# Optimization experiments

Hardware: AMD Instinct MI355X
Metric: run time of the kernel (lower is better)

Reference implementation:

```python
import jax, jax.numpy as jnp
import numpy as np

B, S, DIM, H, HD, K, DEPTH = 2, 2048, 512, 8, 64, 64, 8
SCALE = 1.0 / np.sqrt(HD)


def _cantor_coords(seq_len: int, depth: int) -> np.ndarray:
    # Vectorized port of CantorAttention._cantor_coordinate over all positions.
    x = np.arange(seq_len, dtype=np.float64) / max(1, seq_len - 1)
    x = np.clip(x, 1e-06, 1.0 - 1e-06)
    val = np.zeros(seq_len, dtype=np.float64)
    factor = 0.5
    for _ in range(depth):
        x *= 3.0
        digit = np.floor(x)
        x -= digit
        val += (digit == 2.0) * factor
        factor *= 0.5
    return val.astype(np.float32)


def _build_routes(seq_len: int, k: int, depth: int) -> np.ndarray:
    # k nearest neighbors in Cantor space (smallest |c_i - c_j|), per position.
    c = _cantor_coords(seq_len, depth)
    dist = np.abs(c[:, None] - c[None, :])  # (S, S) built once on host
    routes = np.argsort(dist, axis=1, kind='stable')[:, :k]  # ascending distance
    return routes.astype(np.int32)


def setup_inputs() -> dict:
    key = jax.random.key(0)
    k1, k2, k3 = jax.random.split(key, 3)
    x = jax.random.normal(k1, (B, S, DIM), dtype=jnp.float32)
    Wqkv = jax.random.normal(k2, (DIM, 3 * DIM), dtype=jnp.float32) * (1.0 / np.sqrt(DIM))
    bqkv = jnp.zeros((3 * DIM,), dtype=jnp.float32)
    Wout = jax.random.normal(k3, (DIM, DIM), dtype=jnp.float32) * (1.0 / np.sqrt(DIM))
    bout = jnp.zeros((DIM,), dtype=jnp.float32)
    routes = jnp.asarray(_build_routes(S, K, DEPTH))  # (S, K) int32
    return {"x": x, "Wqkv": Wqkv, "bqkv": bqkv, "Wout": Wout, "bout": bout, "routes": routes}


def reference(x, Wqkv, bqkv, Wout, bout, routes):
    b, s, _ = x.shape
    qkv = x @ Wqkv + bqkv  # (B, S, 3*DIM)
    qkv = qkv.reshape(b, s, 3, H, HD)
    q = jnp.transpose(qkv[:, :, 0], (0, 2, 1, 3))  # (B, H, S, HD)
    k = jnp.transpose(qkv[:, :, 1], (0, 2, 1, 3))
    v = jnp.transpose(qkv[:, :, 2], (0, 2, 1, 3))
    # Gather K/V along sequence dim by Cantor routes -> (B, H, S, K, HD)
    k_g = k[:, :, routes, :]
    v_g = v[:, :, routes, :]
    scores = jnp.einsum('bhsd,bhskd->bhsk', q, k_g) * SCALE
    w = jax.nn.softmax(scores, axis=-1)  # dropout disabled (eval)
    out = jnp.einsum('bhsk,bhskd->bhsd', w, v_g)  # (B, H, S, HD)
    out = jnp.transpose(out, (0, 2, 1, 3)).reshape(b, s, DIM)
    return out @ Wout + bout
```

## Files before the change

kernel.cpp:

```cpp
#include <hip/hip_runtime.h>
#include <math.h>

#define B_    2
#define S_    2048
#define DIM_  512
#define H_    8
#define HD_   64
#define K_    64
#define M_    (B_ * S_)
#define NQKV_ (3 * DIM_)

typedef __attribute__((ext_vector_type(8))) _Float16       half8;
typedef __attribute__((ext_vector_type(2))) _Float16       half2v;
typedef __attribute__((ext_vector_type(8))) unsigned short ushort8v;
typedef __attribute__((ext_vector_type(4))) float          float4v;

__device__ __forceinline__ unsigned short f2h(float f) {
    _Float16 h = (_Float16)f;
    unsigned short u; __builtin_memcpy(&u, &h, 2); return u;
}
__device__ __forceinline__ float h2f(unsigned short u) {
    _Float16 h; __builtin_memcpy(&h, &u, 2); return (float)h;
}

template<int CTRL>
__device__ __forceinline__ float dpp_addf(float x) {
    int y = __builtin_amdgcn_update_dpp(0, __builtin_bit_cast(int, x),
                                        CTRL, 0xF, 0xF, true);
    return x + __builtin_bit_cast(float, y);
}
template<int CTRL>
__device__ __forceinline__ float dpp_maxf(float x) {
    int y = __builtin_amdgcn_update_dpp(0, __builtin_bit_cast(int, x),
                                        CTRL, 0xF, 0xF, true);
    return fmaxf(x, __builtin_bit_cast(float, y));
}

__device__ __forceinline__ void load_lds16(const unsigned short* g, unsigned short* l) {
    __builtin_amdgcn_global_load_lds(
        (const __attribute__((address_space(1))) void*)g,
        (__attribute__((address_space(3))) void*)l, 16, 0, 0);
}

__global__ __launch_bounds__(256) void prep_all(
    const float* __restrict__ X, unsigned short* __restrict__ Xh,
    const float* __restrict__ Wq, unsigned short* __restrict__ Wqh,
    const float* __restrict__ Wo, unsigned short* __restrict__ Woh,
    const int* __restrict__ routes, int* __restrict__ members,
    int4* __restrict__ recs, int* __restrict__ nchp)
{
    __shared__ int smem[2048 * 3 + 256];
    const int bid = blockIdx.x, t = threadIdx.x;

    if (bid < 1024) {
        size_t i = ((size_t)bid * 256 + t) * 8;
        float4 a = *(const float4*)&X[i];
        float4 b = *(const float4*)&X[i + 4];
        float f[8] = {a.x, a.y, a.z, a.w, b.x, b.y, b.z, b.w};
        ushort8v h;
        #pragma unroll
        for (int j = 0; j < 8; ++j) h[j] = f2h(f[j]);
        *(ushort8v*)&Xh[i] = h;
        return;
    }

    if (bid == 2048) {
        int* cnt  = smem;
        int* base = smem + 2048;
        int* cur  = smem + 4096;
        int* ps   = smem + 6144;
        for (int i = t; i < 2048; i += 256) cnt[i] = 0;
        __syncthreads();
        int lead[8];
        #pragma unroll
        for (int i = 0; i < 8; ++i) {
            lead[i] = routes[(size_t)(i * 256 + t) * K_];
            atomicAdd(&cnt[lead[i]], 1);
        }
        __syncthreads();
        int loc[8], sum = 0;
        #pragma unroll
        for (int i = 0; i < 8; ++i) { loc[i] = sum; sum += cnt[t * 8 + i]; }
        ps[t] = sum;
        __syncthreads();
        for (int off = 1; off < 256; off <<= 1) {
            int v = ps[t];
            if (t >= off) v += ps[t - off];
            __syncthreads(); ps[t] = v; __syncthreads();
        }
        const int excl = ps[t] - sum;
        #pragma unroll
        for (int i = 0; i < 8; ++i) { base[t * 8 + i] = excl + loc[i]; cur[t * 8 + i] = 0; }
        __syncthreads();
        #pragma unroll
        for (int i = 0; i < 8; ++i) {
            int s = i * 256 + t;
            members[base[lead[i]] + atomicAdd(&cur[lead[i]], 1)] = s;
        }
        int cloc[8], csum = 0;
        #pragma unroll
        for (int i = 0; i < 8; ++i) { cloc[i] = csum; csum += (cnt[t * 8 + i] + 7) >> 3; }
        __syncthreads();
        ps[t] = csum;
        __syncthreads();
        for (int off = 1; off < 256; off <<= 1) {
            int v = ps[t];
            if (t >= off) v += ps[t - off];
            __syncthreads(); ps[t] = v; __syncthreads();
        }
        const int cexcl = ps[t] - csum;
        #pragma unroll
        for (int i = 0; i < 8; ++i) {
            const int c = t * 8 + i, n = cnt[c];
            int w0 = cexcl + cloc[i];
            for (int k = 0; k * 8 < n; ++k) {
                int rem = n - k * 8;
                recs[w0 + k] = make_int4(c, base[c] + k * 8, rem < 8 ? rem : 8, 0);
            }
        }
        if (t == 255) nchp[0] = ps[255];
        return;
    }

    float (*tile)[33] = (float (*)[33])smem;
    const float* W;
    unsigned short* Whi;
    int N, k0, n0;
    if (bid < 1792) {
        int idx = bid - 1024;
        W = Wq; Whi = Wqh; N = NQKV_;
        n0 = (idx % 48) * 32; k0 = (idx / 48) * 32;
    } else {
        int idx = bid - 1792;
        W = Wo; Whi = Woh; N = DIM_;
        n0 = (idx % 16) * 32; k0 = (idx / 16) * 32;
    }
    const int c = t & 31, r8 = t >> 5;
    #pragma unroll
    for (int i = 0; i < 4; ++i) {
        int r = r8 + i * 8;
        tile[r][c] = W[(size_t)(k0 + r) * N + n0 + c];
    }
    __syncthreads();
    #pragma unroll
    for (int i = 0; i < 4; ++i) {
        int r = r8 + i * 8;
        Whi[(size_t)(n0 + r) * 512 + k0 + c] = f2h(tile[c][r]);
    }
}

template<int BM, int BN, int WM, int WN, int TERMS>
__global__ __launch_bounds__(256) void gemm_mfma(
    const unsigned short* __restrict__ Ahi, const unsigned short* __restrict__ Alo,
    const unsigned short* __restrict__ Wh,
    const float* __restrict__ bias, float* __restrict__ C,
    unsigned short* __restrict__ Qho, unsigned short* __restrict__ Kho,
    unsigned short* __restrict__ Vho,
    int N, int Kd, int mode)
{
    constexpr int TM = WM / 16, TN = WN / 16;
    constexpr int WAVES_N = BN / WN;
    __shared__ unsigned short Ah[2][BM][32];
    __shared__ unsigned short Al[TERMS == 2 ? 2 : 1][TERMS == 2 ? BM : 1][32];
    __shared__ unsigned short Bh[2][BN][32];

    const int t = threadIdx.x, lane = t & 63, wave = t >> 6;
    const int wm = (wave / WAVES_N) * WM, wn = (wave % WAVES_N) * WN;
    const int m0 = blockIdx.y * BM, n0 = blockIdx.x * BN;
    const int l15 = lane & 15, l4 = lane >> 4;

    const int srow = lane >> 2;
    const int scol = (lane & 3) * 8;

    float4v acc[TM][TN];
    #pragma unroll
    for (int i = 0; i < TM; ++i)
        #pragma unroll
        for (int j = 0; j < TN; ++j)
            #pragma unroll
            for (int r = 0; r < 4; ++r) acc[i][j][r] = 0.f;

    const int NK = Kd / 32;

    #pragma unroll
    for (int c = wave; c < BM / 16; c += 4) {
        size_t g = (size_t)(m0 + c * 16 + srow) * Kd + scol;
        load_lds16(&Ahi[g], &Ah[0][c * 16][0]);
        if constexpr (TERMS == 2) load_lds16(&Alo[g], &Al[0][c * 16][0]);
    }
    #pragma unroll
    for (int c = wave; c < BN / 16; c += 4) {
        size_t g = (size_t)(n0 + c * 16 + srow) * Kd + scol;
        load_lds16(&Wh[g], &Bh[0][c * 16][0]);
    }
    __syncthreads();

    for (int ks = 0; ks < NK; ++ks) {
        const int cur = ks & 1, nxt = cur ^ 1;

        if (ks + 1 < NK) {
            const int k1 = (ks + 1) * 32;
            #pragma unroll
            for (int c = wave; c < BM / 16; c += 4) {
                size_t g = (size_t)(m0 + c * 16 + srow) * Kd + k1 + scol;
                load_lds16(&Ahi[g], &Ah[nxt][c * 16][0]);
                if constexpr (TERMS == 2) load_lds16(&Alo[g], &Al[nxt][c * 16][0]);
            }
            #pragma unroll
            for (int c = wave; c < BN / 16; c += 4) {
                size_t g = (size_t)(n0 + c * 16 + srow) * Kd + k1 + scol;
                load_lds16(&Wh[g], &Bh[nxt][c * 16][0]);
            }
        }

        half8 fa_h[TM], fa_l[TM], fb[TN];
        #pragma unroll
        for (int im = 0; im < TM; ++im) {
            fa_h[im] = *(const half8*)&Ah[cur][wm + im * 16 + l15][l4 * 8];
            if constexpr (TERMS == 2)
                fa_l[im] = *(const half8*)&Al[cur][wm + im * 16 + l15][l4 * 8];
        }
        #pragma unroll
        for (int in = 0; in < TN; ++in)
            fb[in] = *(const half8*)&Bh[cur][wn + in * 16 + l15][l4 * 8];
        #pragma unroll
        for (int im = 0; im < TM; ++im)
            #pragma unroll
            for (int in = 0; in < TN; ++in) {
                acc[im][in] = __builtin_amdgcn_mfma_f32_16x16x32_f16(fa_h[im], fb[in], acc[im][in], 0, 0, 0);
                if constexpr (TERMS == 2)
                    acc[im][in] = __builtin_amdgcn_mfma_f32_16x16x32_f16(fa_l[im], fb[in], acc[im][in], 0, 0, 0);
            }

        __syncthreads();
    }

    if (mode == 0) {
        #pragma unroll
        for (int in = 0; in < TN; ++in) {
            int n = n0 + wn + in * 16 + l15;
            float bv = bias[n];
            #pragma unroll
            for (int im = 0; im < TM; ++im) {
                int mb = m0 + wm + im * 16 + l4 * 4;
                #pragma unroll
                for (int r = 0; r < 4; ++r)
                    C[(size_t)(mb + r) * N + n] = acc[im][in][r] + bv;
            }
        }
    } else {
        #pragma unroll
        for (int in = 0; in < TN; ++in) {
            int n = n0 + wn + in * 16 + l15;
            int which = n >> 9, h = (n >> 6) & 7, d = n & 63;
            unsigned short* dst = (which == 0) ? Qho : (which == 1 ? Kho : Vho);
            float bv = bias[n];
            #pragma unroll
            for (int im = 0; im < TM; ++im) {
                int mb = m0 + wm + im * 16 + l4 * 4;
                #pragma unroll
                for (int r = 0; r < 4; ++r) {
                    int m = mb + r, b = m >> 11, s = m & 2047;
                    dst[(((size_t)b * H_ + h) * S_ + s) * HD_ + d] =
                        f2h(acc[im][in][r] + bv);
                }
            }
        }
    }
}

__global__ __launch_bounds__(256, 3) void attn_kernel(
    const unsigned short* __restrict__ Qh, const unsigned short* __restrict__ Kh,
    const unsigned short* __restrict__ Vh, const int* __restrict__ routes,
    const int* __restrict__ members, const int4* __restrict__ recs,
    const int* __restrict__ nchp,
    unsigned short* __restrict__ Oh)
{
    const int wv = threadIdx.x >> 6, lane = threadIdx.x & 63;
    const int p = lane & 7, jl = lane >> 3;

    const int unit = blockIdx.x * 4 + wv;
    const int bh = unit & 15, cidx = unit >> 4;
    const int b = bh >> 3, h = bh & 7;

    const unsigned short* qbase = Qh + (size_t)bh * S_ * HD_;
    const unsigned short* kbase = Kh + (size_t)bh * S_ * HD_;
    const unsigned short* vbase = Vh + (size_t)bh * S_ * HD_;
    const int nch = nchp[0];

    for (int chunk = cidx; chunk < nch; chunk += 512) {
        const int4 rec = recs[chunk];
        const int leader = rec.x, mstart = rec.y, mcnt = rec.z;

        const int rl = routes[(size_t)leader * K_ + lane];

        int mrow[8];
        #pragma unroll
        for (int r = 0; r < 8; ++r)
            mrow[r] = members[mstart + (r < mcnt ? r : 0)];

        ushort8v kreg[8];
        #pragma unroll
        for (int pass = 0; pass < 8; ++pass) {
            int rk = __shfl(rl, pass * 8 + jl);
            kreg[pass] = *(const ushort8v*)&kbase[(size_t)rk * HD_ + p * 8];
        }
        #pragma unroll
        for (int i = 0; i < 8; ++i) asm volatile("" : "+v"(kreg[i]));

        ushort8v vreg[8];
        #pragma unroll
        for (int i = 0; i < 8; ++i) {
            int rv = __shfl(rl, i * 8 + p);
            vreg[i] = *(const ushort8v*)&vbase[(size_t)rv * HD_ + jl * 8];
        }
        #pragma unroll
        for (int i = 0; i < 8; ++i) asm volatile("" : "+v"(vreg[i]));

        half2v q[8][4];
        #pragma unroll
        for (int r = 0; r < 8; ++r) {
            ushort8v qv = *(const ushort8v*)&qbase[(size_t)mrow[r] * HD_ + p * 8];
            __builtin_memcpy(&q[r][0], &qv, 16);
        }

        float sc[8] = {0.f,0.f,0.f,0.f,0.f,0.f,0.f,0.f};
        #pragma unroll
        for (int pass = 0; pass < 8; ++pass) {
            half2v kp[4];
            __builtin_memcpy(kp, &kreg[pass], 16);
            #pragma unroll
            for (int r = 0; r < 8; ++r) {
                float pa = 0.f;
                #pragma unroll
                for (int i = 0; i < 4; ++i)
                    pa = __builtin_amdgcn_fdot2(q[r][i], kp[i], pa, false);
                pa = dpp_addf<0xB1>(pa);
                pa = dpp_addf<0x4E>(pa);
                pa = dpp_addf<0x141>(pa);
                sc[r] = (pass == p) ? pa : sc[r];
            }
        }

        float w[8];
        #pragma unroll
        for (int r = 0; r < 8; ++r) {
            float s = sc[r] * 0.125f;
            float m = s;
            m = dpp_maxf<0xB1>(m);  m = dpp_maxf<0x4E>(m);
            m = dpp_maxf<0x141>(m); m = dpp_maxf<0x140>(m);
            m = fmaxf(m, __shfl_xor(m, 16));
            m = fmaxf(m, __shfl_xor(m, 32));
            float e = __expf(s - m);
            float su = e;
            su = dpp_addf<0xB1>(su);  su = dpp_addf<0x4E>(su);
            su = dpp_addf<0x141>(su); su = dpp_addf<0x140>(su);
            su += __shfl_xor(su, 16);
            su += __shfl_xor(su, 32);
            w[r] = e / su;
        }

        float vf[8][8];
        #pragma unroll
        for (int i = 0; i < 8; ++i)
            #pragma unroll
            for (int j = 0; j < 8; ++j) vf[i][j] = h2f(vreg[i][j]);

        #pragma unroll
        for (int r = 0; r < 8; ++r) {
            float ac[8] = {0.f,0.f,0.f,0.f,0.f,0.f,0.f,0.f};
            #pragma unroll
            for (int i = 0; i < 8; ++i) {
                float wj = __shfl(w[r], p * 8 + i);
                #pragma unroll
                for (int j = 0; j < 8; ++j) ac[j] += wj * vf[i][j];
            }
            #pragma unroll
            for (int j = 0; j < 8; ++j) {
                ac[j] = dpp_addf<0xB1>(ac[j]);
                ac[j] = dpp_addf<0x4E>(ac[j]);
                ac[j] = dpp_addf<0x141>(ac[j]);
            }
            if (p == 0 && r < mcnt) {
                ushort8v ho;
                #pragma unroll
                for (int j = 0; j < 8; ++j) ho[j] = f2h(ac[j]);
                *(ushort8v*)&Oh[((size_t)b * S_ + mrow[r]) * DIM_ + h * HD_ + jl * 8] = ho;
            }
        }
    }
}

extern "C" void kernel_launch(void* const* d_in, const int* in_sizes, int n_in,
                              void* d_out, int out_size, void* d_ws, size_t ws_size,
                              hipStream_t stream)
{
    const float* x      = (const float*)d_in[0];
    const float* Wqkv   = (const float*)d_in[1];
    const float* bqkv   = (const float*)d_in[2];
    const float* Wout   = (const float*)d_in[3];
    const float* bout   = (const float*)d_in[4];
    const int*   routes = (const int*)d_in[5];
    float* out = (float*)d_out;

    char* w = (char*)d_ws;
    unsigned short* Qh = (unsigned short*)(w);
    unsigned short* Kh = (unsigned short*)(w + (8u << 20));
    unsigned short* Vh = (unsigned short*)(w + (16u << 20));
    unsigned short* xh = (unsigned short*)(w + (24u << 20));
    unsigned short* ah = xh;
    unsigned short* wqh = (unsigned short*)(w + (32u << 20));
    unsigned short* woh = (unsigned short*)(w + (32u << 20) + 1572864u);
    int*  members = (int*)(w + (34u << 20));
    int4* recs    = (int4*)(w + (34u << 20) + 8192u);
    int*  nchp    = (int*)(w + (34u << 20) + 8192u + 32768u);

    dim3 blk(256);

    prep_all<<<dim3(2049), blk, 0, stream>>>(x, xh, Wqkv, wqh, Wout, woh,
                                             routes, members, recs, nchp);

    gemm_mfma<128, 96, 64, 48, 1><<<dim3(NQKV_ / 96, M_ / 128), blk, 0, stream>>>(
        xh, nullptr, wqh, bqkv, nullptr, Qh, Kh, Vh, NQKV_, DIM_, 1);

    attn_kernel<<<dim3(2048), blk, 0, stream>>>(Qh, Kh, Vh, routes,
                                                members, recs, nchp, ah);

    gemm_mfma<64, 64, 32, 32, 1><<<dim3(DIM_ / 64, M_ / 64), blk, 0, stream>>>(
        ah, nullptr, woh, bout, out, nullptr, nullptr, nullptr, DIM_, DIM_, 0);
}
```

Measured before the change: 132.7 us.

## Move gathered attention onto MFMA with 16-member chunks and LDS-staged V

The attention kernel now groups up to 16 queries that share a route leader into each chunk, instead of 8. QK^T and PV are computed with 16x16x32 f16 MFMA instructions in place of fdot2 with DPP reductions. The gathered V rows are staged into swizzled LDS through global_load_lds, the probabilities are redistributed with ds_bpermute, and the softmax scale is folded into Q in the QKV GEMM epilogue. The aim is to cut scalar ALU and cross-lane shuffle cost and halve the number of K/V gathers per query. In exchange it adds LDS use, raises the occupancy hint to 4, and writes the output as scattered 2-byte stores.

```diff
diff --git a/kernel.cpp b/kernel.cpp
--- a/kernel.cpp
+++ b/kernel.cpp
@@ -11,29 +11,18 @@
 #define NQKV_ (3 * DIM_)
 
 typedef __attribute__((ext_vector_type(8))) _Float16       half8;
-typedef __attribute__((ext_vector_type(2))) _Float16       half2v;
 typedef __attribute__((ext_vector_type(8))) unsigned short ushort8v;
 typedef __attribute__((ext_vector_type(4))) float          float4v;
+
+union H8 { half8 h; ushort8v u; unsigned int w[4]; };
 
 __device__ __forceinline__ unsigned short f2h(float f) {
     _Float16 h = (_Float16)f;
     unsigned short u; __builtin_memcpy(&u, &h, 2); return u;
 }
-__device__ __forceinline__ float h2f(unsigned short u) {
-    _Float16 h; __builtin_memcpy(&h, &u, 2); return (float)h;
-}
-
-template<int CTRL>
-__device__ __forceinline__ float dpp_addf(float x) {
-    int y = __builtin_amdgcn_update_dpp(0, __builtin_bit_cast(int, x),
-                                        CTRL, 0xF, 0xF, true);
-    return x + __builtin_bit_cast(float, y);
-}
-template<int CTRL>
-__device__ __forceinline__ float dpp_maxf(float x) {
-    int y = __builtin_amdgcn_update_dpp(0, __builtin_bit_cast(int, x),
-                                        CTRL, 0xF, 0xF, true);
-    return fmaxf(x, __builtin_bit_cast(float, y));
+__device__ __forceinline__ unsigned int pkrtz(float a, float b) {
+    auto r = __builtin_amdgcn_cvt_pkrtz(a, b);
+    unsigned int u; __builtin_memcpy(&u, &r, 4); return u;
 }
 
 __device__ __forceinline__ void load_lds16(const unsigned short* g, unsigned short* l) {
@@ -99,7 +88,7 @@
         }
         int cloc[8], csum = 0;
         #pragma unroll
-        for (int i = 0; i < 8; ++i) { cloc[i] = csum; csum += (cnt[t * 8 + i] + 7) >> 3; }
+        for (int i = 0; i < 8; ++i) { cloc[i] = csum; csum += (cnt[t * 8 + i] + 15) >> 4; }
         __syncthreads();
         ps[t] = csum;
         __syncthreads();
@@ -113,9 +102,9 @@
         for (int i = 0; i < 8; ++i) {
             const int c = t * 8 + i, n = cnt[c];
             int w0 = cexcl + cloc[i];
-            for (int k = 0; k * 8 < n; ++k) {
-                int rem = n - k * 8;
-                recs[w0 + k] = make_int4(c, base[c] + k * 8, rem < 8 ? rem : 8, 0);
+            for (int k2 = 0; k2 * 16 < n; ++k2) {
+                int rem = n - k2 * 16;
+                recs[w0 + k2] = make_int4(c, base[c] + k2 * 16, rem < 16 ? rem : 16, 0);
             }
         }
         if (t == 255) nchp[0] = ps[255];
@@ -255,6 +244,7 @@
             int which = n >> 9, h = (n >> 6) & 7, d = n & 63;
             unsigned short* dst = (which == 0) ? Qho : (which == 1 ? Kho : Vho);
             float bv = bias[n];
+            float scl = (which == 0) ? 0.125f : 1.0f;
             #pragma unroll
             for (int im = 0; im < TM; ++im) {
                 int mb = m0 + wm + im * 16 + l4 * 4;
@@ -262,22 +252,23 @@
                 for (int r = 0; r < 4; ++r) {
                     int m = mb + r, b = m >> 11, s = m & 2047;
                     dst[(((size_t)b * H_ + h) * S_ + s) * HD_ + d] =
-                        f2h(acc[im][in][r] + bv);
+                        f2h((acc[im][in][r] + bv) * scl);
                 }
             }
         }
     }
 }
 
-__global__ __launch_bounds__(256, 3) void attn_kernel(
+__global__ __launch_bounds__(256, 4) void attn_kernel(
     const unsigned short* __restrict__ Qh, const unsigned short* __restrict__ Kh,
     const unsigned short* __restrict__ Vh, const int* __restrict__ routes,
     const int* __restrict__ members, const int4* __restrict__ recs,
-    const int* __restrict__ nchp,
-    unsigned short* __restrict__ Oh)
+    const int* __restrict__ nchp, unsigned short* __restrict__ Oh)
 {
+    __shared__ unsigned short VldsAll[4][4096];
     const int wv = threadIdx.x >> 6, lane = threadIdx.x & 63;
-    const int p = lane & 7, jl = lane >> 3;
+    unsigned short* Vlds = VldsAll[wv];
+    const int g = lane >> 4, m16 = lane & 15;
 
     const int unit = blockIdx.x * 4 + wv;
     const int bh = unit & 15, cidx = unit >> 4;
@@ -293,99 +284,112 @@
         const int leader = rec.x, mstart = rec.y, mcnt = rec.z;
 
         const int rl = routes[(size_t)leader * K_ + lane];
-
-        int mrow[8];
-        #pragma unroll
-        for (int r = 0; r < 8; ++r)
-            mrow[r] = members[mstart + (r < mcnt ? r : 0)];
-
-        ushort8v kreg[8];
-        #pragma unroll
-        for (int pass = 0; pass < 8; ++pass) {
-            int rk = __shfl(rl, pass * 8 + jl);
-            kreg[pass] = *(const ushort8v*)&kbase[(size_t)rk * HD_ + p * 8];
-        }
-        #pragma unroll
-        for (int i = 0; i < 8; ++i) asm volatile("" : "+v"(kreg[i]));
-
-        ushort8v vreg[8];
+        const int mm = members[mstart + (m16 < mcnt ? m16 : mcnt - 1)];
+
         #pragma unroll
         for (int i = 0; i < 8; ++i) {
-            int rv = __shfl(rl, i * 8 + p);
-            vreg[i] = *(const ushort8v*)&vbase[(size_t)rv * HD_ + jl * 8];
-        }
-        #pragma unroll
-        for (int i = 0; i < 8; ++i) asm volatile("" : "+v"(vreg[i]));
-
-        half2v q[8][4];
-        #pragma unroll
-        for (int r = 0; r < 8; ++r) {
-            ushort8v qv = *(const ushort8v*)&qbase[(size_t)mrow[r] * HD_ + p * 8];
-            __builtin_memcpy(&q[r][0], &qv, 16);
-        }
-
-        float sc[8] = {0.f,0.f,0.f,0.f,0.f,0.f,0.f,0.f};
-        #pragma unroll
-        for (int pass = 0; pass < 8; ++pass) {
-            half2v kp[4];
-            __builtin_memcpy(kp, &kreg[pass], 16);
-            #pragma unroll
-            for (int r = 0; r < 8; ++r) {
-                float pa = 0.f;
+            int rv = __shfl(rl, i * 8 + (lane >> 3));
+            int sc = (lane & 7) ^ i;
+            load_lds16(&vbase[(size_t)rv * HD_ + sc * 8], Vlds + i * 512);
+        }
+
+        H8 ka[4][2];
+        #pragma unroll
+        for (int tt = 0; tt < 4; ++tt) {
+            int rt = __shfl(rl, tt * 16 + m16);
+            const unsigned short* kr = &kbase[(size_t)rt * HD_];
+            ka[tt][0].u = *(const ushort8v*)(kr + g * 8);
+            ka[tt][1].u = *(const ushort8v*)(kr + 32 + g * 8);
+        }
+        const unsigned short* qr = &qbase[(size_t)mm * HD_];
+        H8 qb0, qb1;
+        qb0.u = *(const ushort8v*)(qr + g * 8);
+        qb1.u = *(const ushort8v*)(qr + 32 + g * 8);
+
+        float4v acc[4];
+        #pragma unroll
+        for (int tt = 0; tt < 4; ++tt) {
+            #pragma unroll
+            for (int r = 0; r < 4; ++r) acc[tt][r] = 0.f;
+        }
+        #pragma unroll
+        for (int tt = 0; tt < 4; ++tt) {
+            acc[tt] = __builtin_amdgcn_mfma_f32_16x16x32_f16(ka[tt][0].h, qb0.h, acc[tt], 0, 0, 0);
+            acc[tt] = __builtin_amdgcn_mfma_f32_16x16x32_f16(ka[tt][1].h, qb1.h, acc[tt], 0, 0, 0);
+        }
+
+        float mx = acc[0][0];
+        #pragma unroll
+        for (int tt = 0; tt < 4; ++tt)
+            #pragma unroll
+            for (int r = 0; r < 4; ++r) mx = fmaxf(mx, acc[tt][r]);
+        mx = fmaxf(mx, __shfl_xor(mx, 16));
+        mx = fmaxf(mx, __shfl_xor(mx, 32));
+        float ew[4][4], su = 0.f;
+        #pragma unroll
+        for (int tt = 0; tt < 4; ++tt)
+            #pragma unroll
+            for (int r = 0; r < 4; ++r) { ew[tt][r] = __expf(acc[tt][r] - mx); su += ew[tt][r]; }
+        su += __shfl_xor(su, 16);
+        su += __shfl_xor(su, 32);
+        const float rinv = __builtin_amdgcn_rcpf(su);
+
+        unsigned int whu[4][2];
+        #pragma unroll
+        for (int tt = 0; tt < 4; ++tt) {
+            whu[tt][0] = pkrtz(ew[tt][0] * rinv, ew[tt][1] * rinv);
+            whu[tt][1] = pkrtz(ew[tt][2] * rinv, ew[tt][3] * rinv);
+        }
+
+        const int A0 = (((g & 1) << 5) | m16) * 4;
+        const int A1 = A0 + 64;
+        const bool ghi = (g >> 1) != 0;
+        H8 pa[2];
+        #pragma unroll
+        for (int s = 0; s < 2; ++s) {
+            unsigned int l0a = (unsigned int)__builtin_amdgcn_ds_bpermute(A0, (int)whu[2 * s][0]);
+            unsigned int l0b = (unsigned int)__builtin_amdgcn_ds_bpermute(A0, (int)whu[2 * s + 1][0]);
+            unsigned int h0a = (unsigned int)__builtin_amdgcn_ds_bpermute(A0, (int)whu[2 * s][1]);
+            unsigned int h0b = (unsigned int)__builtin_amdgcn_ds_bpermute(A0, (int)whu[2 * s + 1][1]);
+            unsigned int l1a = (unsigned int)__builtin_amdgcn_ds_bpermute(A1, (int)whu[2 * s][0]);
+            unsigned int l1b = (unsigned int)__builtin_amdgcn_ds_bpermute(A1, (int)whu[2 * s + 1][0]);
+            unsigned int h1a = (unsigned int)__builtin_amdgcn_ds_bpermute(A1, (int)whu[2 * s][1]);
+            unsigned int h1b = (unsigned int)__builtin_amdgcn_ds_bpermute(A1, (int)whu[2 * s + 1][1]);
+            pa[s].w[0] = ghi ? l0b : l0a;
+            pa[s].w[1] = ghi ? h0b : h0a;
+            pa[s].w[2] = ghi ? l1b : l1a;
+            pa[s].w[3] = ghi ? h1b : h1a;
+        }
+
+        int mr[4];
+        #pragma unroll
+        for (int r = 0; r < 4; ++r)
+            mr[r] = __builtin_amdgcn_ds_bpermute((g * 4 + r) * 4, mm);
+
+        asm volatile("s_waitcnt vmcnt(0)" ::: "memory");
+        __builtin_amdgcn_sched_barrier(0);
+
+        #pragma unroll
+        for (int dblk = 0; dblk < 4; ++dblk) {
+            H8 vb[2];
+            #pragma unroll
+            for (int s = 0; s < 2; ++s) {
+                const char* vp = (const char*)Vlds + (s * 32 + g * 8) * 128 +
+                    (((dblk * 16 + m16) * 2) ^ ((((s * 4 + g) & 7)) << 4));
                 #pragma unroll
-                for (int i = 0; i < 4; ++i)
-                    pa = __builtin_amdgcn_fdot2(q[r][i], kp[i], pa, false);
-                pa = dpp_addf<0xB1>(pa);
-                pa = dpp_addf<0x4E>(pa);
-                pa = dpp_addf<0x141>(pa);
-                sc[r] = (pass == p) ? pa : sc[r];
-            }
-        }
-
-        float w[8];
-        #pragma unroll
-        for (int r = 0; r < 8; ++r) {
-            float s = sc[r] * 0.125f;
-            float m = s;
-            m = dpp_maxf<0xB1>(m);  m = dpp_maxf<0x4E>(m);
-            m = dpp_maxf<0x141>(m); m = dpp_maxf<0x140>(m);
-            m = fmaxf(m, __shfl_xor(m, 16));
-            m = fmaxf(m, __shfl_xor(m, 32));
-            float e = __expf(s - m);
-            float su = e;
-            su = dpp_addf<0xB1>(su);  su = dpp_addf<0x4E>(su);
-            su = dpp_addf<0x141>(su); su = dpp_addf<0x140>(su);
-            su += __shfl_xor(su, 16);
-            su += __shfl_xor(su, 32);
-            w[r] = e / su;
-        }
-
-        float vf[8][8];
-        #pragma unroll
-        for (int i = 0; i < 8; ++i)
-            #pragma unroll
-            for (int j = 0; j < 8; ++j) vf[i][j] = h2f(vreg[i][j]);
-
-        #pragma unroll
-        for (int r = 0; r < 8; ++r) {
-            float ac[8] = {0.f,0.f,0.f,0.f,0.f,0.f,0.f,0.f};
-            #pragma unroll
-            for (int i = 0; i < 8; ++i) {
-                float wj = __shfl(w[r], p * 8 + i);
-                #pragma unroll
-                for (int j = 0; j < 8; ++j) ac[j] += wj * vf[i][j];
-            }
-            #pragma unroll
-            for (int j = 0; j < 8; ++j) {
-                ac[j] = dpp_addf<0xB1>(ac[j]);
-                ac[j] = dpp_addf<0x4E>(ac[j]);
-                ac[j] = dpp_addf<0x141>(ac[j]);
-            }
-            if (p == 0 && r < mcnt) {
-                ushort8v ho;
-                #pragma unroll
-                for (int j = 0; j < 8; ++j) ho[j] = f2h(ac[j]);
-                *(ushort8v*)&Oh[((size_t)b * S_ + mrow[r]) * DIM_ + h * HD_ + jl * 8] = ho;
+                for (int j = 0; j < 8; ++j)
+                    vb[s].u[j] = *(const unsigned short*)(vp + j * 128);
+            }
+            float4v o;
+            o[0] = 0.f; o[1] = 0.f; o[2] = 0.f; o[3] = 0.f;
+            o = __builtin_amdgcn_mfma_f32_16x16x32_f16(pa[0].h, vb[0].h, o, 0, 0, 0);
+            o = __builtin_amdgcn_mfma_f32_16x16x32_f16(pa[1].h, vb[1].h, o, 0, 0, 0);
+            #pragma unroll
+            for (int r = 0; r < 4; ++r) {
+                if (g * 4 + r < mcnt) {
+                    size_t oi = ((size_t)b * S_ + mr[r]) * DIM_ + h * HD_ + dblk * 16 + m16;
+                    Oh[oi] = f2h(o[r]);
+                }
             }
         }
     }
```

Measured after the change: 118.1 us. 11.0% less time.
